# Performance work log

Measured on AMD Instinct MI355X. Metric: run time of the kernel, lower is better.

Reference implementation:

```python
import jax, jax.numpy as jnp
import numpy as np

H = 64          # hidden_dim
TF = 24         # forecast_length


def _a_norm(N):
    # Complete graph (all i!=j) + GCNConv default self-loops => A+I = ones(N,N).
    # deg_i = N, so D^-1/2 (A+I) D^-1/2 = ones / N. Built generically below.
    A = jnp.ones((N, N), dtype=jnp.float32)
    deg = A.sum(axis=1)
    return A / jnp.sqrt(deg[:, None] * deg[None, :])


def _gcn(x, A, W, b):
    # PyG GCNConv: aggregate(norm * (x W)) + bias
    return jnp.einsum('ij,...jh->...ih', A, x @ W) + b


def setup_inputs() -> dict:
    key = jax.random.key(0)
    ks = jax.random.split(key, 20)
    B, N, T = 32, 128, 96
    s = lambda k, shape, fan: (jax.random.normal(k, shape, jnp.float32) / np.sqrt(max(fan, 1)))
    return {
        'x': jax.random.normal(ks[0], (B, N, T), jnp.float32),
        # spatial GCN stack
        'W_s1': s(ks[1], (1, H), 1), 'b_s1': jnp.zeros((H,), jnp.float32),
        'W_s2': s(ks[2], (H, H), H), 'b_s2': jnp.zeros((H,), jnp.float32),
        # temporal attention MLP
        'Wa1': s(ks[3], (H, H), H), 'ba1': jnp.zeros((H,), jnp.float32),
        'Wa2': s(ks[4], (H, 1), H), 'ba2': jnp.zeros((1,), jnp.float32),
        # GRU (single step, h0 = 0)
        'W_ih': s(ks[5], (3 * H, H), H), 'W_hh': s(ks[6], (3 * H, H), H),
        'b_ih': jnp.zeros((3 * H,), jnp.float32), 'b_hh': jnp.zeros((3 * H,), jnp.float32),
        # ODE-func GCN stack
        'W_o1': s(ks[7], (H, H), H), 'b_o1': jnp.zeros((H,), jnp.float32),
        'W_o2': s(ks[8], (H, H), H), 'b_o2': jnp.zeros((H,), jnp.float32),
        # output head
        'W_out': s(ks[9], (H, 1), H), 'b_out': jnp.zeros((1,), jnp.float32),
    }


def reference(x, W_s1, b_s1, W_s2, b_s2, Wa1, ba1, Wa2, ba2,
              W_ih, W_hh, b_ih, b_hh, W_o1, b_o1, W_o2, b_o2, W_out, b_out):
    B, N, T = x.shape
    A = _a_norm(N)

    # --- spatial encoding, vectorized over (batch, time) ---
    xt = jnp.transpose(x, (0, 2, 1))[..., None]          # (B, T, N, 1)
    h = jax.nn.relu(_gcn(xt, A, W_s1, b_s1))             # (B, T, N, H)
    h = jax.nn.relu(_gcn(h, A, W_s2, b_s2))

    # --- temporal attention over time axis ---
    att = jnp.tanh(h @ Wa1 + ba1) @ Wa2 + ba2            # (B, T, N, 1)
    w = jax.nn.softmax(att, axis=1)
    nf = jnp.sum(h * w, axis=1)                          # (B, N, H)

    # --- one-step GRU encoder with zero initial hidden ---
    gi = nf.reshape(B * N, -1) @ W_ih.T + b_ih           # (B*N, 3H)
    gi_r, gi_z, gi_n = jnp.split(gi, 3, axis=-1)
    bh_r, bh_z, bh_n = jnp.split(b_hh, 3)
    r = jax.nn.sigmoid(gi_r + bh_r)
    z = jax.nn.sigmoid(gi_z + bh_z)
    n = jnp.tanh(gi_n + r * bh_n)
    hidden = ((1.0 - z) * n).reshape(B, N, -1)           # (B, N, H)

    # --- graph ODE derivative: two GCN layers + tanh ---
    def f(y):
        y = jnp.tanh(_gcn(y, A, W_o1, b_o1))
        y = jnp.tanh(_gcn(y, A, W_o2, b_o2))
        return y

    # torchdiffeq fixed-grid 'rk4' (3/8 rule) on t = linspace(0, TF, TF)
    dt = jnp.float32(TF / (TF - 1))
    third = jnp.float32(1.0 / 3.0)

    def step(y, _):
        k1 = f(y)
        k2 = f(y + dt * k1 * third)
        k3 = f(y + dt * (k2 - k1 * third))
        k4 = f(y + dt * (k1 - k2 + k3))
        y1 = y + dt * (k1 + 3.0 * (k2 + k3) + k4) * jnp.float32(0.125)
        return y1, y1

    _, ys = jax.lax.scan(step, hidden, None, length=TF - 1)
    traj = jnp.concatenate([hidden[None], ys], axis=0)   # (TF, B, N, H)

    # output head then rearrange to (B, N, TF)
    preds = (traj @ W_out + b_out)[..., 0]               # (TF, B, N)
    return jnp.transpose(preds, (1, 2, 0))
```

## Files before the change

kernel.cpp:

```cpp
#include <hip/hip_runtime.h>


#define BN 32
#define NN 128
#define TT 96
#define HH 64
#define TFC 24

#if defined(__has_builtin)
#if __has_builtin(__builtin_amdgcn_fdot2)
#define HAVE_FDOT2 1
#endif
#if __has_builtin(__builtin_amdgcn_update_dpp)
#define HAVE_DPP 1
#endif
#endif

using half2v = __fp16 __attribute__((ext_vector_type(2)));

__device__ __forceinline__ unsigned pack_pair(float a, float b) {
    union { half2v h; unsigned u; } c;
    c.h = __builtin_amdgcn_cvt_pkrtz(a, b);
    return c.u;
}
__device__ __forceinline__ half2v as_h2(unsigned u) {
    union { unsigned u; half2v h; } c; c.u = u; return c.h;
}
__device__ __forceinline__ unsigned rdlu(unsigned v, int l) {
    return (unsigned)__builtin_amdgcn_readlane((int)v, l);
}
__device__ __forceinline__ float rdl(float v, int l) {
    return __int_as_float(__builtin_amdgcn_readlane(__float_as_int(v), l));
}

template <int CTRL>
__device__ __forceinline__ float dppf(float x) {
#if HAVE_DPP
    return __int_as_float(
        __builtin_amdgcn_update_dpp(0, __float_as_int(x), CTRL, 0xF, 0xF, true));
#else
    return 0.f;
#endif
}

__device__ __forceinline__ float xor1(float x) {
#if HAVE_DPP
    return dppf<0xB1>(x);
#else
    return __shfl_xor(x, 1, 64);
#endif
}

__device__ __forceinline__ float wave_sum(float v) {
#if HAVE_DPP
    v += dppf<0xB1>(v);
    v += dppf<0x4E>(v);
    v += dppf<0x141>(v);
    v += dppf<0x140>(v);
    return ((rdl(v, 0) + rdl(v, 16)) + (rdl(v, 32) + rdl(v, 48)));
#else
#pragma unroll
    for (int off = 32; off > 0; off >>= 1) v += __shfl_xor(v, off, 64);
    return v;
#endif
}
__device__ __forceinline__ void wave_sum2(float& a, float& b) {
#if HAVE_DPP
    a += dppf<0xB1>(a);  b += dppf<0xB1>(b);
    a += dppf<0x4E>(a);  b += dppf<0x4E>(b);
    a += dppf<0x141>(a); b += dppf<0x141>(b);
    a += dppf<0x140>(a); b += dppf<0x140>(b);
    a = (rdl(a, 0) + rdl(a, 16)) + (rdl(a, 32) + rdl(a, 48));
    b = (rdl(b, 0) + rdl(b, 16)) + (rdl(b, 32) + rdl(b, 48));
#else
    a = wave_sum(a); b = wave_sum(b);
#endif
}
__device__ __forceinline__ float wave_max(float v) {
#if HAVE_DPP
    v = fmaxf(v, dppf<0xB1>(v));
    v = fmaxf(v, dppf<0x4E>(v));
    v = fmaxf(v, dppf<0x141>(v));
    v = fmaxf(v, dppf<0x140>(v));
    return fmaxf(fmaxf(rdl(v, 0), rdl(v, 16)), fmaxf(rdl(v, 32), rdl(v, 48)));
#else
#pragma unroll
    for (int off = 32; off > 0; off >>= 1) v = fmaxf(v, __shfl_xor(v, off, 64));
    return v;
#endif
}

__device__ __forceinline__ float dot2acc(unsigned w, unsigned up, float acc) {
#if HAVE_FDOT2
    return __builtin_amdgcn_fdot2(as_h2(w), as_h2(up), acc, false);
#else
    const half2v wh = as_h2(w), uh = as_h2(up);
    return fmaf((float)wh.y, (float)uh.y, fmaf((float)wh.x, (float)uh.x, acc));
#endif
}

#define PMV64(WP, UPACK, RES)                                              \
    do {                                                                   \
        float c0 = 0.f, c1 = 0.f, c2 = 0.f, c3 = 0.f;                      \
        _Pragma("unroll")                                                  \
        for (int k = 0; k < 32; k += 8) {                                  \
            const unsigned u0 = rdlu(UPACK, 2 * k);                        \
            const unsigned u1 = rdlu(UPACK, 2 * k + 2);                    \
            const unsigned u2 = rdlu(UPACK, 2 * k + 4);                    \
            const unsigned u3 = rdlu(UPACK, 2 * k + 6);                    \
            const unsigned u4 = rdlu(UPACK, 2 * k + 8);                    \
            const unsigned u5 = rdlu(UPACK, 2 * k + 10);                   \
            const unsigned u6 = rdlu(UPACK, 2 * k + 12);                   \
            const unsigned u7 = rdlu(UPACK, 2 * k + 14);                   \
            c0 = dot2acc(WP[k],     u0, c0);                               \
            c1 = dot2acc(WP[k + 1], u1, c1);                               \
            c2 = dot2acc(WP[k + 2], u2, c2);                               \
            c3 = dot2acc(WP[k + 3], u3, c3);                               \
            c0 = dot2acc(WP[k + 4], u4, c0);                               \
            c1 = dot2acc(WP[k + 5], u5, c1);                               \
            c2 = dot2acc(WP[k + 6], u6, c2);                               \
            c3 = dot2acc(WP[k + 7], u7, c3);                               \
        }                                                                  \
        RES = (c0 + c1) + (c2 + c3);                                       \
    } while (0)

#define PMV64_2(WP, UA, UB, RA, RB)                                        \
    do {                                                                   \
        float a0 = 0.f, a1 = 0.f, a2 = 0.f, a3 = 0.f;                      \
        float b0 = 0.f, b1 = 0.f, b2 = 0.f, b3 = 0.f;                      \
        _Pragma("unroll")                                                  \
        for (int k = 0; k < 32; k += 4) {                                  \
            const unsigned ua0 = rdlu(UA, 2 * k);                          \
            const unsigned ub0 = rdlu(UB, 2 * k);                          \
            const unsigned ua1 = rdlu(UA, 2 * k + 2);                      \
            const unsigned ub1 = rdlu(UB, 2 * k + 2);                      \
            const unsigned ua2 = rdlu(UA, 2 * k + 4);                      \
            const unsigned ub2 = rdlu(UB, 2 * k + 4);                      \
            const unsigned ua3 = rdlu(UA, 2 * k + 6);                      \
            const unsigned ub3 = rdlu(UB, 2 * k + 6);                      \
            a0 = dot2acc(WP[k],     ua0, a0);                              \
            b0 = dot2acc(WP[k],     ub0, b0);                              \
            a1 = dot2acc(WP[k + 1], ua1, a1);                              \
            b1 = dot2acc(WP[k + 1], ub1, b1);                              \
            a2 = dot2acc(WP[k + 2], ua2, a2);                              \
            b2 = dot2acc(WP[k + 2], ub2, b2);                              \
            a3 = dot2acc(WP[k + 3], ua3, a3);                              \
            b3 = dot2acc(WP[k + 3], ub3, b3);                              \
        }                                                                  \
        RA = (a0 + a1) + (a2 + a3);                                        \
        RB = (b0 + b1) + (b2 + b3);                                        \
    } while (0)

__device__ __forceinline__ float fast_tanh(float x) {
    float e = __expf(2.f * x);
    return 1.f - 2.f * __builtin_amdgcn_rcpf(e + 1.f);
}
__device__ __forceinline__ float fast_sigmoid(float x) {
    return __builtin_amdgcn_rcpf(1.f + __expf(-x));
}

__global__ __launch_bounds__(256)
__attribute__((amdgpu_waves_per_eu(1, 1)))
void fused_kernel(
    const float* __restrict__ x,    const float* __restrict__ Ws1,
    const float* __restrict__ bs1,  const float* __restrict__ Ws2,
    const float* __restrict__ bs2,  const float* __restrict__ Wa1,
    const float* __restrict__ ba1,  const float* __restrict__ Wa2,
    const float* __restrict__ Wih,  const float* __restrict__ bih,
    const float* __restrict__ bhh,  const float* __restrict__ Wo1,
    const float* __restrict__ bo1p, const float* __restrict__ Wo2,
    const float* __restrict__ bo2p, const float* __restrict__ Wout,
    const float* __restrict__ boutp, float* __restrict__ out)
{
    const int tid  = threadIdx.x;
    const int lane = tid & 63;
    const int w    = tid >> 6;
    const int b    = blockIdx.x;

    __shared__ float xbar[TT];
    __shared__ float h2s[TT][HH];
    __shared__ float atts[TT];

    if (tid < TT) {
        const float* xb = x + (size_t)b * NN * TT + tid;
        float s = 0.f;
#pragma unroll
        for (int n = 0; n < NN; ++n) s += xb[n * TT];
        xbar[tid] = s * (1.f / 128.f);
    }

    {
        const float ws1l = Ws1[lane];
        const float bs1l = bs1[lane];
        const float bs2l = bs2[lane];
        const float ba1l = ba1[lane];
        const float wa2l = Wa2[lane];
        unsigned ws2p[32], wa1p[32];
#pragma unroll
        for (int k = 0; k < 32; ++k) {
            ws2p[k] = pack_pair(Ws2[(2 * k) * HH + lane], Ws2[(2 * k + 1) * HH + lane]);
            wa1p[k] = pack_pair(Wa1[(2 * k) * HH + lane], Wa1[(2 * k + 1) * HH + lane]);
        }
#pragma unroll
        for (int k = 0; k < 32; ++k) {
            asm volatile("" : "+v"(ws2p[k]), "+v"(wa1p[k]));
        }
        __syncthreads();

#pragma unroll 1
        for (int i = 0; i < TT / 8; ++i) {
            const int t0 = w * (TT / 4) + 2 * i;
            const int t1 = t0 + 1;
            const float sA = xbar[t0];
            const float sB = xbar[t1];
            const float h1A = fmaxf(fmaf(sA, ws1l, bs1l), 0.f);
            const float h1B = fmaxf(fmaf(sB, ws1l, bs1l), 0.f);
            const unsigned uA = pack_pair(h1A, xor1(h1A));
            const unsigned uB = pack_pair(h1B, xor1(h1B));
            float accA, accB;
            PMV64_2(ws2p, uA, uB, accA, accB);
            const float h2A = fmaxf(accA + bs2l, 0.f);
            const float h2B = fmaxf(accB + bs2l, 0.f);
            h2s[t0][lane] = h2A;
            h2s[t1][lane] = h2B;

            const unsigned vA = pack_pair(h2A, xor1(h2A));
            const unsigned vB = pack_pair(h2B, xor1(h2B));
            PMV64_2(wa1p, vA, vB, accA, accB);
            float gA = fast_tanh(accA + ba1l) * wa2l;
            float gB = fast_tanh(accB + ba1l) * wa2l;
            wave_sum2(gA, gB);
            if (lane == 0) { atts[t0] = gA; atts[t1] = gB; }
        }
    }
    __syncthreads();

    if (w != 0) return;

    const float a0s = atts[lane];
    const float a1s = (lane < TT - 64) ? atts[64 + lane] : -1e30f;
    const float m = wave_max(fmaxf(a0s, a1s));
    const float e0 = __expf(a0s - m);
    const float e1 = (lane < TT - 64) ? __expf(a1s - m) : 0.f;
    const float inv = __builtin_amdgcn_rcpf(wave_sum(e0 + e1));
    const float q0 = e0 * inv;
    const float q1 = e1 * inv;

    float nf = 0.f;
#pragma unroll
    for (int t = 0; t < 64; ++t) nf = fmaf(rdl(q0, t), h2s[t][lane], nf);
#pragma unroll
    for (int t = 0; t < 32; ++t) nf = fmaf(rdl(q1, t), h2s[64 + t][lane], nf);

    float gr = bih[lane];
    float gz = bih[64 + lane];
    float gn = bih[128 + lane];
#pragma unroll
    for (int j = 0; j < HH; j += 4) {
        const float4 wr = *(const float4*)&Wih[(size_t)lane * HH + j];
        const float4 wz = *(const float4*)&Wih[(size_t)(64 + lane) * HH + j];
        const float4 wn = *(const float4*)&Wih[(size_t)(128 + lane) * HH + j];
        const float n0 = rdl(nf, j), n1 = rdl(nf, j + 1);
        const float n2 = rdl(nf, j + 2), n3 = rdl(nf, j + 3);
        gr += n0 * wr.x + n1 * wr.y + n2 * wr.z + n3 * wr.w;
        gz += n0 * wz.x + n1 * wz.y + n2 * wz.z + n3 * wz.w;
        gn += n0 * wn.x + n1 * wn.y + n2 * wn.z + n3 * wn.w;
    }
    const float r = fast_sigmoid(gr + bhh[lane]);
    const float z = fast_sigmoid(gz + bhh[64 + lane]);
    const float n = fast_tanh(gn + r * bhh[128 + lane]);
    float y = (1.f - z) * n;

    unsigned w1p[32], w2p[32];
#pragma unroll
    for (int k = 0; k < 32; ++k) {
        w1p[k] = pack_pair(Wo1[(2 * k) * HH + lane], Wo1[(2 * k + 1) * HH + lane]);
        w2p[k] = pack_pair(Wo2[(2 * k) * HH + lane], Wo2[(2 * k + 1) * HH + lane]);
    }
#pragma unroll
    for (int k = 0; k < 32; ++k) {
        asm volatile("" : "+v"(w1p[k]), "+v"(w2p[k]));
    }
    const float bo1 = bo1p[lane];
    const float bo2 = bo2p[lane];
    const float wo  = Wout[lane];
    const float bo  = boutp[0];

    auto f_eval = [&](float u) -> float {
        const unsigned upA = pack_pair(u, xor1(u));
        float acc;
        PMV64(w1p, upA, acc);
        const float v = fast_tanh(acc + bo1);
        const unsigned upB = pack_pair(v, xor1(v));
        PMV64(w2p, upB, acc);
        return fast_tanh(acc + bo2);
    };

    float* ob = out + (size_t)b * NN * TFC;
    {
        const float p = wave_sum(y * wo) + bo;
        ob[lane * TFC]        = p;
        ob[(64 + lane) * TFC] = p;
    }

    const float dt = (float)(24.0 / 23.0);
    const float third = 1.f / 3.f;

#pragma unroll 1
    for (int st = 0; st < TFC - 1; ++st) {
        const float k1 = f_eval(y);
        const float k2 = f_eval(y + dt * k1 * third);
        const float k3 = f_eval(y + dt * (k2 - k1 * third));
        const float k4 = f_eval(y + dt * (k1 - k2 + k3));
        y = y + dt * (k1 + 3.f * (k2 + k3) + k4) * 0.125f;
        const float p = wave_sum(y * wo) + bo;
        ob[lane * TFC + st + 1]        = p;
        ob[(64 + lane) * TFC + st + 1] = p;
    }
}

extern "C" void kernel_launch(void* const* d_in, const int* in_sizes, int n_in,
                              void* d_out, int out_size, void* d_ws, size_t ws_size,
                              hipStream_t stream) {
    (void)in_sizes; (void)n_in; (void)d_ws; (void)ws_size; (void)out_size;
    const float* x    = (const float*)d_in[0];
    const float* Ws1  = (const float*)d_in[1];
    const float* bs1  = (const float*)d_in[2];
    const float* Ws2  = (const float*)d_in[3];
    const float* bs2  = (const float*)d_in[4];
    const float* Wa1  = (const float*)d_in[5];
    const float* ba1  = (const float*)d_in[6];
    const float* Wa2  = (const float*)d_in[7];
    const float* Wih  = (const float*)d_in[9];
    const float* bih  = (const float*)d_in[11];
    const float* bhh  = (const float*)d_in[12];
    const float* Wo1  = (const float*)d_in[13];
    const float* bo1  = (const float*)d_in[14];
    const float* Wo2  = (const float*)d_in[15];
    const float* bo2  = (const float*)d_in[16];
    const float* Wout = (const float*)d_in[17];
    const float* bout = (const float*)d_in[18];

    fused_kernel<<<dim3(BN), dim3(256), 0, stream>>>(
        x, Ws1, bs1, Ws2, bs2, Wa1, ba1, Wa2,
        Wih, bih, bhh, Wo1, bo1, Wo2, bo2, Wout, bout,
        (float*)d_out);
}
```

Baseline: 132.5 us.

## Process two batches per block to interleave serial ODE matvec chains

Each block now handles two batch elements. The ODE integration runs both batches' matvecs together through the paired PMV64_2 macro, so two independent dependency chains are interleaved on the one wave that does the serial RK4 loop. The grid is halved to 16 blocks and each wave's spatial encoding now covers 48 timesteps of one batch. This trades parallelism across CUs, and doubles the per-block encoder work, for better instruction-level parallelism and weight reuse in the latency-bound recurrence.

```diff
diff --git a/kernel.cpp b/kernel.cpp
--- a/kernel.cpp
+++ b/kernel.cpp
@@ -98,31 +98,6 @@
     return fmaf((float)wh.y, (float)uh.y, fmaf((float)wh.x, (float)uh.x, acc));
 #endif
 }
-
-#define PMV64(WP, UPACK, RES)                                              \
-    do {                                                                   \
-        float c0 = 0.f, c1 = 0.f, c2 = 0.f, c3 = 0.f;                      \
-        _Pragma("unroll")                                                  \
-        for (int k = 0; k < 32; k += 8) {                                  \
-            const unsigned u0 = rdlu(UPACK, 2 * k);                        \
-            const unsigned u1 = rdlu(UPACK, 2 * k + 2);                    \
-            const unsigned u2 = rdlu(UPACK, 2 * k + 4);                    \
-            const unsigned u3 = rdlu(UPACK, 2 * k + 6);                    \
-            const unsigned u4 = rdlu(UPACK, 2 * k + 8);                    \
-            const unsigned u5 = rdlu(UPACK, 2 * k + 10);                   \
-            const unsigned u6 = rdlu(UPACK, 2 * k + 12);                   \
-            const unsigned u7 = rdlu(UPACK, 2 * k + 14);                   \
-            c0 = dot2acc(WP[k],     u0, c0);                               \
-            c1 = dot2acc(WP[k + 1], u1, c1);                               \
-            c2 = dot2acc(WP[k + 2], u2, c2);                               \
-            c3 = dot2acc(WP[k + 3], u3, c3);                               \
-            c0 = dot2acc(WP[k + 4], u4, c0);                               \
-            c1 = dot2acc(WP[k + 5], u5, c1);                               \
-            c2 = dot2acc(WP[k + 6], u6, c2);                               \
-            c3 = dot2acc(WP[k + 7], u7, c3);                               \
-        }                                                                  \
-        RES = (c0 + c1) + (c2 + c3);                                       \
-    } while (0)
 
 #define PMV64_2(WP, UA, UB, RA, RB)                                        \
     do {                                                                   \
@@ -159,8 +134,7 @@
     return __builtin_amdgcn_rcpf(1.f + __expf(-x));
 }
 
-__global__ __launch_bounds__(256)
-__attribute__((amdgpu_waves_per_eu(1, 1)))
+__global__ __launch_bounds__(256, 1)
 void fused_kernel(
     const float* __restrict__ x,    const float* __restrict__ Ws1,
     const float* __restrict__ bs1,  const float* __restrict__ Ws2,
@@ -175,18 +149,21 @@
     const int tid  = threadIdx.x;
     const int lane = tid & 63;
     const int w    = tid >> 6;
-    const int b    = blockIdx.x;
-
-    __shared__ float xbar[TT];
-    __shared__ float h2s[TT][HH];
-    __shared__ float atts[TT];
-
-    if (tid < TT) {
-        const float* xb = x + (size_t)b * NN * TT + tid;
+    const int b0   = 2 * blockIdx.x;
+    const int b1   = b0 + 1;
+
+    __shared__ float xbar2[2][TT];
+    __shared__ float h2s[2][TT][HH];
+    __shared__ float atts[2][TT];
+
+    if (tid < 2 * TT) {
+        const int bi = tid / TT;
+        const int t  = tid - bi * TT;
+        const float* xb = x + (size_t)(b0 + bi) * NN * TT + t;
         float s = 0.f;
 #pragma unroll
         for (int n = 0; n < NN; ++n) s += xb[n * TT];
-        xbar[tid] = s * (1.f / 128.f);
+        xbar2[bi][t] = s * (1.f / 128.f);
     }
 
     {
@@ -207,12 +184,14 @@
         }
         __syncthreads();
 
+        const int bb = w >> 1;
+        const int tb = (w & 1) * 48;
 #pragma unroll 1
-        for (int i = 0; i < TT / 8; ++i) {
-            const int t0 = w * (TT / 4) + 2 * i;
+        for (int i = 0; i < 24; ++i) {
+            const int t0 = tb + 2 * i;
             const int t1 = t0 + 1;
-            const float sA = xbar[t0];
-            const float sB = xbar[t1];
+            const float sA = xbar2[bb][t0];
+            const float sB = xbar2[bb][t1];
             const float h1A = fmaxf(fmaf(sA, ws1l, bs1l), 0.f);
             const float h1B = fmaxf(fmaf(sB, ws1l, bs1l), 0.f);
             const unsigned uA = pack_pair(h1A, xor1(h1A));
@@ -221,8 +200,8 @@
             PMV64_2(ws2p, uA, uB, accA, accB);
             const float h2A = fmaxf(accA + bs2l, 0.f);
             const float h2B = fmaxf(accB + bs2l, 0.f);
-            h2s[t0][lane] = h2A;
-            h2s[t1][lane] = h2B;
+            h2s[bb][t0][lane] = h2A;
+            h2s[bb][t1][lane] = h2B;
 
             const unsigned vA = pack_pair(h2A, xor1(h2A));
             const unsigned vB = pack_pair(h2B, xor1(h2B));
@@ -230,46 +209,51 @@
             float gA = fast_tanh(accA + ba1l) * wa2l;
             float gB = fast_tanh(accB + ba1l) * wa2l;
             wave_sum2(gA, gB);
-            if (lane == 0) { atts[t0] = gA; atts[t1] = gB; }
+            if (lane == 0) { atts[bb][t0] = gA; atts[bb][t1] = gB; }
         }
     }
     __syncthreads();
 
     if (w != 0) return;
 
-    const float a0s = atts[lane];
-    const float a1s = (lane < TT - 64) ? atts[64 + lane] : -1e30f;
-    const float m = wave_max(fmaxf(a0s, a1s));
-    const float e0 = __expf(a0s - m);
-    const float e1 = (lane < TT - 64) ? __expf(a1s - m) : 0.f;
-    const float inv = __builtin_amdgcn_rcpf(wave_sum(e0 + e1));
-    const float q0 = e0 * inv;
-    const float q1 = e1 * inv;
-
-    float nf = 0.f;
-#pragma unroll
-    for (int t = 0; t < 64; ++t) nf = fmaf(rdl(q0, t), h2s[t][lane], nf);
-#pragma unroll
-    for (int t = 0; t < 32; ++t) nf = fmaf(rdl(q1, t), h2s[64 + t][lane], nf);
-
-    float gr = bih[lane];
-    float gz = bih[64 + lane];
-    float gn = bih[128 + lane];
-#pragma unroll
-    for (int j = 0; j < HH; j += 4) {
-        const float4 wr = *(const float4*)&Wih[(size_t)lane * HH + j];
-        const float4 wz = *(const float4*)&Wih[(size_t)(64 + lane) * HH + j];
-        const float4 wn = *(const float4*)&Wih[(size_t)(128 + lane) * HH + j];
-        const float n0 = rdl(nf, j), n1 = rdl(nf, j + 1);
-        const float n2 = rdl(nf, j + 2), n3 = rdl(nf, j + 3);
-        gr += n0 * wr.x + n1 * wr.y + n2 * wr.z + n3 * wr.w;
-        gz += n0 * wz.x + n1 * wz.y + n2 * wz.z + n3 * wz.w;
-        gn += n0 * wn.x + n1 * wn.y + n2 * wn.z + n3 * wn.w;
-    }
-    const float r = fast_sigmoid(gr + bhh[lane]);
-    const float z = fast_sigmoid(gz + bhh[64 + lane]);
-    const float n = fast_tanh(gn + r * bhh[128 + lane]);
-    float y = (1.f - z) * n;
+    float yv[2];
+#pragma unroll 1
+    for (int bi = 0; bi < 2; ++bi) {
+        const float a0s = atts[bi][lane];
+        const float a1s = (lane < TT - 64) ? atts[bi][64 + lane] : -1e30f;
+        const float m = wave_max(fmaxf(a0s, a1s));
+        const float e0 = __expf(a0s - m);
+        const float e1 = (lane < TT - 64) ? __expf(a1s - m) : 0.f;
+        const float inv = __builtin_amdgcn_rcpf(wave_sum(e0 + e1));
+        const float q0 = e0 * inv;
+        const float q1 = e1 * inv;
+
+        float nf = 0.f;
+#pragma unroll
+        for (int t = 0; t < 64; ++t) nf = fmaf(rdl(q0, t), h2s[bi][t][lane], nf);
+#pragma unroll
+        for (int t = 0; t < 32; ++t) nf = fmaf(rdl(q1, t), h2s[bi][64 + t][lane], nf);
+
+        float gr = bih[lane];
+        float gz = bih[64 + lane];
+        float gn = bih[128 + lane];
+#pragma unroll
+        for (int j = 0; j < HH; j += 4) {
+            const float4 wr = *(const float4*)&Wih[(size_t)lane * HH + j];
+            const float4 wz = *(const float4*)&Wih[(size_t)(64 + lane) * HH + j];
+            const float4 wn = *(const float4*)&Wih[(size_t)(128 + lane) * HH + j];
+            const float n0 = rdl(nf, j), n1 = rdl(nf, j + 1);
+            const float n2 = rdl(nf, j + 2), n3 = rdl(nf, j + 3);
+            gr += n0 * wr.x + n1 * wr.y + n2 * wr.z + n3 * wr.w;
+            gz += n0 * wz.x + n1 * wz.y + n2 * wz.z + n3 * wz.w;
+            gn += n0 * wn.x + n1 * wn.y + n2 * wn.z + n3 * wn.w;
+        }
+        const float r = fast_sigmoid(gr + bhh[lane]);
+        const float z = fast_sigmoid(gz + bhh[64 + lane]);
+        const float n = fast_tanh(gn + r * bhh[128 + lane]);
+        yv[bi] = (1.f - z) * n;
+    }
+    float y0 = yv[0], y1 = yv[1];
 
     unsigned w1p[32], w2p[32];
 #pragma unroll
@@ -286,21 +270,30 @@
     const float wo  = Wout[lane];
     const float bo  = boutp[0];
 
-    auto f_eval = [&](float u) -> float {
-        const unsigned upA = pack_pair(u, xor1(u));
-        float acc;
-        PMV64(w1p, upA, acc);
-        const float v = fast_tanh(acc + bo1);
-        const unsigned upB = pack_pair(v, xor1(v));
-        PMV64(w2p, upB, acc);
-        return fast_tanh(acc + bo2);
+    auto f_eval2 = [&](float uA, float uB, float& rA, float& rB) {
+        const unsigned pA = pack_pair(uA, xor1(uA));
+        const unsigned pB = pack_pair(uB, xor1(uB));
+        float aA, aB;
+        PMV64_2(w1p, pA, pB, aA, aB);
+        const float vA = fast_tanh(aA + bo1);
+        const float vB = fast_tanh(aB + bo1);
+        const unsigned qA = pack_pair(vA, xor1(vA));
+        const unsigned qB = pack_pair(vB, xor1(vB));
+        PMV64_2(w2p, qA, qB, aA, aB);
+        rA = fast_tanh(aA + bo2);
+        rB = fast_tanh(aB + bo2);
     };
 
-    float* ob = out + (size_t)b * NN * TFC;
+    float* ob0 = out + (size_t)b0 * NN * TFC;
+    float* ob1 = out + (size_t)b1 * NN * TFC;
     {
-        const float p = wave_sum(y * wo) + bo;
-        ob[lane * TFC]        = p;
-        ob[(64 + lane) * TFC] = p;
+        float p0 = y0 * wo, p1 = y1 * wo;
+        wave_sum2(p0, p1);
+        p0 += bo; p1 += bo;
+        ob0[lane * TFC]        = p0;
+        ob0[(64 + lane) * TFC] = p0;
+        ob1[lane * TFC]        = p1;
+        ob1[(64 + lane) * TFC] = p1;
     }
 
     const float dt = (float)(24.0 / 23.0);
@@ -308,14 +301,22 @@
 
 #pragma unroll 1
     for (int st = 0; st < TFC - 1; ++st) {
-        const float k1 = f_eval(y);
-        const float k2 = f_eval(y + dt * k1 * third);
-        const float k3 = f_eval(y + dt * (k2 - k1 * third));
-        const float k4 = f_eval(y + dt * (k1 - k2 + k3));
-        y = y + dt * (k1 + 3.f * (k2 + k3) + k4) * 0.125f;
-        const float p = wave_sum(y * wo) + bo;
-        ob[lane * TFC + st + 1]        = p;
-        ob[(64 + lane) * TFC + st + 1] = p;
+        float k1A, k1B, k2A, k2B, k3A, k3B, k4A, k4B;
+        f_eval2(y0, y1, k1A, k1B);
+        f_eval2(y0 + dt * k1A * third, y1 + dt * k1B * third, k2A, k2B);
+        f_eval2(y0 + dt * (k2A - k1A * third), y1 + dt * (k2B - k1B * third),
+                k3A, k3B);
+        f_eval2(y0 + dt * (k1A - k2A + k3A), y1 + dt * (k1B - k2B + k3B),
+                k4A, k4B);
+        y0 = y0 + dt * (k1A + 3.f * (k2A + k3A) + k4A) * 0.125f;
+        y1 = y1 + dt * (k1B + 3.f * (k2B + k3B) + k4B) * 0.125f;
+        float p0 = y0 * wo, p1 = y1 * wo;
+        wave_sum2(p0, p1);
+        p0 += bo; p1 += bo;
+        ob0[lane * TFC + st + 1]        = p0;
+        ob0[(64 + lane) * TFC + st + 1] = p0;
+        ob1[lane * TFC + st + 1]        = p1;
+        ob1[(64 + lane) * TFC + st + 1] = p1;
     }
 }
 
@@ -341,7 +342,7 @@
     const float* Wout = (const float*)d_in[17];
     const float* bout = (const float*)d_in[18];
 
-    fused_kernel<<<dim3(BN), dim3(256), 0, stream>>>(
+    fused_kernel<<<dim3(BN / 2), dim3(256), 0, stream>>>(
         x, Ws1, bs1, Ws2, bs2, Wa1, ba1, Wa2,
         Wih, bih, bhh, Wo1, bo1, Wo2, bo2, Wout, bout,
         (float*)d_out);
```

New measurement: 165.4 us. +24.9%, slower.

## Split fused kernel into parallel spatial kernel and single-wave ODE kernel

Applied to the files above, without the earlier changes.

Splits the single fused kernel into two launches. A spatial/attention kernel spreads the time axis over four blocks per batch, so 128 blocks run instead of 32, and writes packed fp16 h2 and attention scores to workspace. A 64-thread ODE kernel then reads them, does the softmax pooling with fp16 dot2, and runs the GRU and RK4 loop. PMV64 is also restructured to hoist all lane reads ahead of the dot products. The cost is a second launch, a round trip through global memory, and fp16 rounding of the h2 values.

```diff
diff --git a/kernel.cpp b/kernel.cpp
--- a/kernel.cpp
+++ b/kernel.cpp
@@ -101,25 +101,16 @@
 
 #define PMV64(WP, UPACK, RES)                                              \
     do {                                                                   \
+        unsigned us_[32];                                                  \
+        _Pragma("unroll")                                                  \
+        for (int k = 0; k < 32; ++k) us_[k] = rdlu(UPACK, 2 * k);          \
         float c0 = 0.f, c1 = 0.f, c2 = 0.f, c3 = 0.f;                      \
         _Pragma("unroll")                                                  \
-        for (int k = 0; k < 32; k += 8) {                                  \
-            const unsigned u0 = rdlu(UPACK, 2 * k);                        \
-            const unsigned u1 = rdlu(UPACK, 2 * k + 2);                    \
-            const unsigned u2 = rdlu(UPACK, 2 * k + 4);                    \
-            const unsigned u3 = rdlu(UPACK, 2 * k + 6);                    \
-            const unsigned u4 = rdlu(UPACK, 2 * k + 8);                    \
-            const unsigned u5 = rdlu(UPACK, 2 * k + 10);                   \
-            const unsigned u6 = rdlu(UPACK, 2 * k + 12);                   \
-            const unsigned u7 = rdlu(UPACK, 2 * k + 14);                   \
-            c0 = dot2acc(WP[k],     u0, c0);                               \
-            c1 = dot2acc(WP[k + 1], u1, c1);                               \
-            c2 = dot2acc(WP[k + 2], u2, c2);                               \
-            c3 = dot2acc(WP[k + 3], u3, c3);                               \
-            c0 = dot2acc(WP[k + 4], u4, c0);                               \
-            c1 = dot2acc(WP[k + 5], u5, c1);                               \
-            c2 = dot2acc(WP[k + 6], u6, c2);                               \
-            c3 = dot2acc(WP[k + 7], u7, c3);                               \
+        for (int k = 0; k < 32; k += 4) {                                  \
+            c0 = dot2acc(WP[k],     us_[k],     c0);                       \
+            c1 = dot2acc(WP[k + 1], us_[k + 1], c1);                       \
+            c2 = dot2acc(WP[k + 2], us_[k + 2], c2);                       \
+            c3 = dot2acc(WP[k + 3], us_[k + 3], c3);                       \
         }                                                                  \
         RES = (c0 + c1) + (c2 + c3);                                       \
     } while (0)
@@ -159,86 +150,90 @@
     return __builtin_amdgcn_rcpf(1.f + __expf(-x));
 }
 
-__global__ __launch_bounds__(256)
-__attribute__((amdgpu_waves_per_eu(1, 1)))
-void fused_kernel(
+__global__ __launch_bounds__(256) void spatial_kernel(
     const float* __restrict__ x,    const float* __restrict__ Ws1,
     const float* __restrict__ bs1,  const float* __restrict__ Ws2,
     const float* __restrict__ bs2,  const float* __restrict__ Wa1,
     const float* __restrict__ ba1,  const float* __restrict__ Wa2,
+    unsigned* __restrict__ ws_h2,   float* __restrict__ ws_att)
+{
+    const int tid  = threadIdx.x;
+    const int lane = tid & 63;
+    const int w    = tid >> 6;
+    const int tq   = blockIdx.x;
+    const int b    = blockIdx.y;
+    const int tbase = tq * 24;
+
+    __shared__ float xbar[24];
+    if (tid < 24) {
+        const float* xb = x + (size_t)b * NN * TT + (tbase + tid);
+        float s = 0.f;
+#pragma unroll
+        for (int n = 0; n < NN; ++n) s += xb[n * TT];
+        xbar[tid] = s * (1.f / 128.f);
+    }
+
+    const float ws1l = Ws1[lane];
+    const float bs1l = bs1[lane];
+    const float bs2l = bs2[lane];
+    const float ba1l = ba1[lane];
+    const float wa2l = Wa2[lane];
+    unsigned ws2p[32], wa1p[32];
+#pragma unroll
+    for (int k = 0; k < 32; ++k) {
+        ws2p[k] = pack_pair(Ws2[(2 * k) * HH + lane], Ws2[(2 * k + 1) * HH + lane]);
+        wa1p[k] = pack_pair(Wa1[(2 * k) * HH + lane], Wa1[(2 * k + 1) * HH + lane]);
+    }
+#pragma unroll
+    for (int k = 0; k < 32; ++k) {
+        asm volatile("" : "+v"(ws2p[k]), "+v"(wa1p[k]));
+    }
+    __syncthreads();
+
+#pragma unroll 1
+    for (int i = 0; i < 3; ++i) {
+        const int tl0 = w * 6 + 2 * i;
+        const float sA = xbar[tl0];
+        const float sB = xbar[tl0 + 1];
+        const float h1A = fmaxf(fmaf(sA, ws1l, bs1l), 0.f);
+        const float h1B = fmaxf(fmaf(sB, ws1l, bs1l), 0.f);
+        const unsigned uA = pack_pair(h1A, xor1(h1A));
+        const unsigned uB = pack_pair(h1B, xor1(h1B));
+        float accA, accB;
+        PMV64_2(ws2p, uA, uB, accA, accB);
+        const float h2A = fmaxf(accA + bs2l, 0.f);
+        const float h2B = fmaxf(accB + bs2l, 0.f);
+        ws_h2[((size_t)b * (TT / 2) + (tbase + tl0) / 2) * HH + lane] =
+            pack_pair(h2A, h2B);
+
+        const unsigned vA = pack_pair(h2A, xor1(h2A));
+        const unsigned vB = pack_pair(h2B, xor1(h2B));
+        PMV64_2(wa1p, vA, vB, accA, accB);
+        float gA = fast_tanh(accA + ba1l) * wa2l;
+        float gB = fast_tanh(accB + ba1l) * wa2l;
+        wave_sum2(gA, gB);
+        if (lane == 0) {
+            ws_att[b * TT + tbase + tl0]     = gA;
+            ws_att[b * TT + tbase + tl0 + 1] = gB;
+        }
+    }
+}
+
+__global__ __launch_bounds__(64)
+__attribute__((amdgpu_waves_per_eu(1, 1)))
+void ode_kernel(
+    const unsigned* __restrict__ ws_h2, const float* __restrict__ ws_att,
     const float* __restrict__ Wih,  const float* __restrict__ bih,
     const float* __restrict__ bhh,  const float* __restrict__ Wo1,
     const float* __restrict__ bo1p, const float* __restrict__ Wo2,
     const float* __restrict__ bo2p, const float* __restrict__ Wout,
     const float* __restrict__ boutp, float* __restrict__ out)
 {
-    const int tid  = threadIdx.x;
-    const int lane = tid & 63;
-    const int w    = tid >> 6;
+    const int lane = threadIdx.x;
     const int b    = blockIdx.x;
 
-    __shared__ float xbar[TT];
-    __shared__ float h2s[TT][HH];
-    __shared__ float atts[TT];
-
-    if (tid < TT) {
-        const float* xb = x + (size_t)b * NN * TT + tid;
-        float s = 0.f;
-#pragma unroll
-        for (int n = 0; n < NN; ++n) s += xb[n * TT];
-        xbar[tid] = s * (1.f / 128.f);
-    }
-
-    {
-        const float ws1l = Ws1[lane];
-        const float bs1l = bs1[lane];
-        const float bs2l = bs2[lane];
-        const float ba1l = ba1[lane];
-        const float wa2l = Wa2[lane];
-        unsigned ws2p[32], wa1p[32];
-#pragma unroll
-        for (int k = 0; k < 32; ++k) {
-            ws2p[k] = pack_pair(Ws2[(2 * k) * HH + lane], Ws2[(2 * k + 1) * HH + lane]);
-            wa1p[k] = pack_pair(Wa1[(2 * k) * HH + lane], Wa1[(2 * k + 1) * HH + lane]);
-        }
-#pragma unroll
-        for (int k = 0; k < 32; ++k) {
-            asm volatile("" : "+v"(ws2p[k]), "+v"(wa1p[k]));
-        }
-        __syncthreads();
-
-#pragma unroll 1
-        for (int i = 0; i < TT / 8; ++i) {
-            const int t0 = w * (TT / 4) + 2 * i;
-            const int t1 = t0 + 1;
-            const float sA = xbar[t0];
-            const float sB = xbar[t1];
-            const float h1A = fmaxf(fmaf(sA, ws1l, bs1l), 0.f);
-            const float h1B = fmaxf(fmaf(sB, ws1l, bs1l), 0.f);
-            const unsigned uA = pack_pair(h1A, xor1(h1A));
-            const unsigned uB = pack_pair(h1B, xor1(h1B));
-            float accA, accB;
-            PMV64_2(ws2p, uA, uB, accA, accB);
-            const float h2A = fmaxf(accA + bs2l, 0.f);
-            const float h2B = fmaxf(accB + bs2l, 0.f);
-            h2s[t0][lane] = h2A;
-            h2s[t1][lane] = h2B;
-
-            const unsigned vA = pack_pair(h2A, xor1(h2A));
-            const unsigned vB = pack_pair(h2B, xor1(h2B));
-            PMV64_2(wa1p, vA, vB, accA, accB);
-            float gA = fast_tanh(accA + ba1l) * wa2l;
-            float gB = fast_tanh(accB + ba1l) * wa2l;
-            wave_sum2(gA, gB);
-            if (lane == 0) { atts[t0] = gA; atts[t1] = gB; }
-        }
-    }
-    __syncthreads();
-
-    if (w != 0) return;
-
-    const float a0s = atts[lane];
-    const float a1s = (lane < TT - 64) ? atts[64 + lane] : -1e30f;
+    const float a0s = ws_att[b * TT + lane];
+    const float a1s = (lane < TT - 64) ? ws_att[b * TT + 64 + lane] : -1e30f;
     const float m = wave_max(fmaxf(a0s, a1s));
     const float e0 = __expf(a0s - m);
     const float e1 = (lane < TT - 64) ? __expf(a1s - m) : 0.f;
@@ -246,11 +241,21 @@
     const float q0 = e0 * inv;
     const float q1 = e1 * inv;
 
+    const unsigned* h2b = ws_h2 + (size_t)b * (TT / 2) * HH;
+    unsigned hp[TT / 2];
+#pragma unroll
+    for (int tp = 0; tp < TT / 2; ++tp) hp[tp] = h2b[tp * HH + lane];
     float nf = 0.f;
 #pragma unroll
-    for (int t = 0; t < 64; ++t) nf = fmaf(rdl(q0, t), h2s[t][lane], nf);
-#pragma unroll
-    for (int t = 0; t < 32; ++t) nf = fmaf(rdl(q1, t), h2s[64 + t][lane], nf);
+    for (int tp = 0; tp < 32; ++tp) {
+        const unsigned qp = pack_pair(rdl(q0, 2 * tp), rdl(q0, 2 * tp + 1));
+        nf = dot2acc(hp[tp], qp, nf);
+    }
+#pragma unroll
+    for (int tp = 32; tp < TT / 2; ++tp) {
+        const unsigned qp = pack_pair(rdl(q1, 2 * tp - 64), rdl(q1, 2 * tp - 63));
+        nf = dot2acc(hp[tp], qp, nf);
+    }
 
     float gr = bih[lane];
     float gz = bih[64 + lane];
@@ -322,7 +327,7 @@
 extern "C" void kernel_launch(void* const* d_in, const int* in_sizes, int n_in,
                               void* d_out, int out_size, void* d_ws, size_t ws_size,
                               hipStream_t stream) {
-    (void)in_sizes; (void)n_in; (void)d_ws; (void)ws_size; (void)out_size;
+    (void)in_sizes; (void)n_in; (void)ws_size; (void)out_size;
     const float* x    = (const float*)d_in[0];
     const float* Ws1  = (const float*)d_in[1];
     const float* bs1  = (const float*)d_in[2];
@@ -341,8 +346,13 @@
     const float* Wout = (const float*)d_in[17];
     const float* bout = (const float*)d_in[18];
 
-    fused_kernel<<<dim3(BN), dim3(256), 0, stream>>>(
-        x, Ws1, bs1, Ws2, bs2, Wa1, ba1, Wa2,
-        Wih, bih, bhh, Wo1, bo1, Wo2, bo2, Wout, bout,
+    unsigned* ws_h2 = (unsigned*)d_ws;
+    float* ws_att   = (float*)((char*)d_ws + (size_t)BN * (TT / 2) * HH * 4);
+
+    spatial_kernel<<<dim3(4, BN), dim3(256), 0, stream>>>(
+        x, Ws1, bs1, Ws2, bs2, Wa1, ba1, Wa2, ws_h2, ws_att);
+
+    ode_kernel<<<dim3(BN), dim3(64), 0, stream>>>(
+        ws_h2, ws_att, Wih, bih, bhh, Wo1, bo1, Wo2, bo2, Wout, bout,
         (float*)d_out);
 }
```

Measured after the change: 125.2 us. 1.06x faster.
